# Kernel tuning notes

Hardware: AMD Instinct MI355X
Metric: run time of the kernel (lower is better)

## Reference

```python
import jax, jax.numpy as jnp
import numpy as np

NPOINT = 1024
RADIUS = 0.2
NSAMPLE = 32


def furthest_point_sampling(xyz, npoint):
    # xyz: (B, N, 3) -> (B, npoint) int32 indices
    B, N, _ = xyz.shape

    def step(carry, _):
        dist, far = carry
        centroid = jnp.take_along_axis(xyz, far[:, None, None], axis=1)  # (B,1,3)
        d = jnp.sum((xyz - centroid) ** 2, axis=-1)                       # (B,N)
        dist = jnp.minimum(dist, d)
        new_far = jnp.argmax(dist, axis=-1).astype(jnp.int32)
        return (dist, new_far), far

    init = (jnp.full((B, N), 1e10, xyz.dtype), jnp.zeros((B,), jnp.int32))
    _, idx = jax.lax.scan(step, init, None, length=npoint)
    return idx.T  # (B, npoint)


def ball_query(xyz, new_xyz, radius, nsample):
    # xyz: (B,N,3), new_xyz: (B,S,3) -> (B,S,nsample) int32 indices
    N = xyz.shape[1]
    d2 = jnp.sum((new_xyz[:, :, None, :] - xyz[:, None, :, :]) ** 2, axis=-1)  # (B,S,N)
    # pick first `nsample` indices within radius (CUDA ball_query semantics)
    key = jnp.where(d2 < radius * radius, jnp.arange(N, dtype=jnp.int32)[None, None, :], N)
    idx = jnp.sort(key, axis=-1)[..., :nsample]          # (B,S,nsample)
    first = idx[..., :1]
    idx = jnp.where(idx == N, first, idx)                # pad with first valid
    return jnp.clip(idx, 0, N - 1).astype(jnp.int32)     # guard empty balls


def sa_forward(xyz, features, W1, s1, b1, W2, s2, b2, W3, s3, b3):
    B, N, _ = xyz.shape
    center_idx = furthest_point_sampling(xyz, NPOINT)                     # (B,S)
    new_xyz = jnp.take_along_axis(xyz, center_idx[..., None], axis=1)     # (B,S,3)

    idx = ball_query(xyz, new_xyz, RADIUS, NSAMPLE)                       # (B,S,K)
    # group xyz (relative coords) and features
    g_xyz = jnp.take_along_axis(xyz[:, None], idx[..., None], axis=2)     # (B,S,K,3)
    g_xyz = g_xyz - new_xyz[:, :, None, :]
    feats_n = jnp.swapaxes(features, 1, 2)                                # (B,N,C)
    g_feat = jnp.take_along_axis(feats_n[:, None], idx[..., None], axis=2)  # (B,S,K,C)
    g = jnp.concatenate([g_xyz, g_feat], axis=-1)                         # (B,S,K,3+C)
    x = jnp.transpose(g, (0, 3, 1, 2))                                    # (B,3+C,S,K)

    # 1x1 conv MLP with (folded) BN affine + ReLU
    for W, s, b in ((W1, s1, b1), (W2, s2, b2), (W3, s3, b3)):
        x = jax.nn.relu(jnp.einsum('oi,bisk->bosk', W, x)
                        * s[None, :, None, None] + b[None, :, None, None])
    new_features = jnp.max(x, axis=-1)                                    # (B,Cout,S)
    return new_xyz, new_features


def setup_inputs() -> dict:
    key = jax.random.key(0)
    ks = jax.random.split(key, 11)
    B, N, C = 4, 16384, 64
    return {
        'xyz': jax.random.uniform(ks[0], (B, N, 3), jnp.float32),
        'features': jax.random.normal(ks[1], (B, C, N), jnp.float32),
        'W1': jax.random.normal(ks[2], (64, C + 3), jnp.float32) * 0.1,
        's1': jax.random.uniform(ks[3], (64,), jnp.float32),
        'b1': jax.random.normal(ks[4], (64,), jnp.float32) * 0.1,
        'W2': jax.random.normal(ks[5], (64, 64), jnp.float32) * 0.1,
        's2': jax.random.uniform(ks[6], (64,), jnp.float32),
        'b2': jax.random.normal(ks[7], (64,), jnp.float32) * 0.1,
        'W3': jax.random.normal(ks[8], (128, 64), jnp.float32) * 0.1,
        's3': jax.random.uniform(ks[9], (128,), jnp.float32),
        'b3': jax.random.normal(ks[10], (128,), jnp.float32) * 0.1,
    }


def reference(xyz, features, W1, s1, b1, W2, s2, b2, W3, s3, b3):
    return sa_forward(xyz, features, W1, s1, b1, W2, s2, b2, W3, s3, b3)
```

## Files before the change

### kernel.cpp

```cpp
#include <hip/hip_runtime.h>
#include <cstdint>
#include <cstddef>

#define BATCH   4
#define NPTS    16384
#define NPOINT  1024
#define NSAMPLE 32
#define CIN     67
#define R2f     0.04f

#define FPS_T   512
#define FPS_P   32

#define RPT32(M) M(0)M(1)M(2)M(3)M(4)M(5)M(6)M(7)M(8)M(9)M(10)M(11)M(12)M(13)M(14)M(15) \
                 M(16)M(17)M(18)M(19)M(20)M(21)M(22)M(23)M(24)M(25)M(26)M(27)M(28)M(29)M(30)M(31)

template <int CTRL, int RMASK>
__device__ __forceinline__ void amax_dpp(float& v, int& i) {
  int nv = __builtin_amdgcn_update_dpp(__float_as_int(v), __float_as_int(v),
                                       CTRL, RMASK, 0xf, false);
  int ni = __builtin_amdgcn_update_dpp(i, i, CTRL, RMASK, 0xf, false);
  float fv = __int_as_float(nv);
  bool tk = (fv > v) || (fv == v && ni < i);
  v = tk ? fv : v;
  i = tk ? ni : i;
}

__global__ void __attribute__((amdgpu_flat_work_group_size(FPS_T, FPS_T),
                               amdgpu_waves_per_eu(2, 2)))
fps_kernel(const float* __restrict__ xyz, float* __restrict__ out_newxyz)
{
  const int b = blockIdx.x;
  const float* base = xyz + (size_t)b * NPTS * 3;
  const int t = threadIdx.x;
  const int lane = t & 63, w = t >> 6;

#define DECLV(i) float px##i, py##i, pz##i, dd##i;
  RPT32(DECLV)
#undef DECLV
#define LOADV(i) { const float* p = base + (size_t)(((i) << 9) + t) * 3; \
                   px##i = p[0]; py##i = p[1]; pz##i = p[2]; dd##i = 1e10f; }
  RPT32(LOADV)
#undef LOADV

  __shared__ float s_wv[2][8];
  __shared__ int   s_wi[2][8];

  float cx = base[0], cy = base[1], cz = base[2];

  for (int it = 0; it < NPOINT; ++it) {
    if (t == 0) {
      int o = (b * NPOINT + it) * 3;
      out_newxyz[o + 0] = cx;
      out_newxyz[o + 1] = cy;
      out_newxyz[o + 2] = cz;
    }
    float bv = -1.0f; int bl = 0;
#define STEPV(i) { \
    float dx = __fsub_rn(px##i, cx); \
    float dy = __fsub_rn(py##i, cy); \
    float dz = __fsub_rn(pz##i, cz); \
    float d2 = __fadd_rn(__fadd_rn(__fmul_rn(dx, dx), __fmul_rn(dy, dy)), \
                         __fmul_rn(dz, dz)); \
    float nd = fminf(dd##i, d2); dd##i = nd; \
    bool tk = nd > bv;   \
    bv = tk ? nd : bv; \
    bl = tk ? (i) : bl; }
    RPT32(STEPV)
#undef STEPV
    int bi = (bl << 9) + t;

    amax_dpp<0x121, 0xf>(bv, bi);
    amax_dpp<0x122, 0xf>(bv, bi);
    amax_dpp<0x124, 0xf>(bv, bi);
    amax_dpp<0x128, 0xf>(bv, bi);
    amax_dpp<0x142, 0xa>(bv, bi);
    amax_dpp<0x143, 0xc>(bv, bi);

    const int par = it & 1;
    if (lane == 63) { s_wv[par][w] = bv; s_wi[par][w] = bi; }
    __syncthreads();

    float gv = s_wv[par][lane & 7];
    int   gi = s_wi[par][lane & 7];
    amax_dpp<0x121, 0xf>(gv, gi);
    amax_dpp<0x122, 0xf>(gv, gi);
    amax_dpp<0x124, 0xf>(gv, gi);

    int far = __builtin_amdgcn_readfirstlane(gi);
    cx = base[far * 3 + 0];
    cy = base[far * 3 + 1];
    cz = base[far * 3 + 2];
  }
}

__global__ __launch_bounds__(256) void transpose_kernel(
    const float* __restrict__ f, float* __restrict__ ft)
{
  __shared__ float tile[64][65];
  int b  = blockIdx.x >> 8;
  int n0 = (blockIdx.x & 255) << 6;
  for (int v = threadIdx.x; v < 64 * 64; v += 256) {
    int c = v >> 6, j = v & 63;
    tile[c][j] = f[((size_t)(b * 64 + c)) * NPTS + n0 + j];
  }
  __syncthreads();
  for (int v = threadIdx.x; v < 64 * 64; v += 256) {
    int j = v >> 6, c = v & 63;
    ft[((size_t)(b * NPTS + n0 + j)) * 64 + c] = tile[c][j];
  }
}

__global__ __launch_bounds__(1024) void mlp_kernel(
    const float* __restrict__ xyz,
    const float* __restrict__ feats,
    const float* __restrict__ featsT,
    const float* __restrict__ nx,
    const float* __restrict__ W1, const float* __restrict__ s1, const float* __restrict__ b1,
    const float* __restrict__ W2, const float* __restrict__ s2, const float* __restrict__ b2,
    const float* __restrict__ W3, const float* __restrict__ s3, const float* __restrict__ b3,
    float* __restrict__ outF)
{
  __shared__ float W1t[CIN * 64];
  __shared__ float W2t[64 * 64];
  __shared__ float sb[512];
  __shared__ float xs[CIN * 34];
  __shared__ float h1[64 * 34];
  __shared__ float h2[64 * 34];
  __shared__ int   hm[128];
  __shared__ int   lid8[8][NSAMPLE];

  const int tid = threadIdx.x;
  const int lane = tid & 63, w = tid >> 6;

  for (int v = tid; v < CIN * 64; v += 1024) {
    int o = v / CIN, i = v - o * CIN;
    W1t[i * 64 + o] = W1[v];
  }
  for (int v = tid; v < 64 * 64; v += 1024) {
    int o = v >> 6, i = v & 63;
    W2t[i * 64 + o] = W2[v];
  }
  if (tid < 64)       sb[tid]       = s1[tid];
  else if (tid < 128) sb[tid]       = b1[tid - 64];
  else if (tid < 192) sb[tid]       = s2[tid - 128];
  else if (tid < 256) sb[tid]       = b2[tid - 192];
  else if (tid < 384) sb[tid]       = s3[tid - 256];
  else if (tid < 512) sb[tid]       = b3[tid - 384];

  if (w < 8) {
    int g = (blockIdx.x << 3) + w;
    int b = g >> 10;
    const float* base = xyz + (size_t)b * NPTS * 3;
    float cx = nx[g * 3 + 0], cy = nx[g * 3 + 1], cz = nx[g * 3 + 2];
    int cnt = 0, fidx = -1;
    for (int c0 = 0; c0 < NPTS && cnt < NSAMPLE; c0 += 64) {
      int i = c0 + lane;
      float dx = __fsub_rn(base[i * 3 + 0], cx);
      float dy = __fsub_rn(base[i * 3 + 1], cy);
      float dz = __fsub_rn(base[i * 3 + 2], cz);
      float d2 = __fadd_rn(__fadd_rn(__fmul_rn(dx, dx), __fmul_rn(dy, dy)),
                           __fmul_rn(dz, dz));
      bool pred = d2 < R2f;
      unsigned long long mk = __ballot(pred);
      if (pred) {
        int rank = cnt + __popcll(mk & ((1ull << lane) - 1ull));
        if (rank < NSAMPLE) lid8[w][rank] = i;
        if (rank == 0) fidx = i;
      }
      cnt += __popcll(mk);
    }
#pragma unroll
    for (int off = 32; off >= 1; off >>= 1) {
      int o = __shfl_xor(fidx, off);
      fidx = o > fidx ? o : fidx;
    }
    if (lane >= cnt && lane < NSAMPLE) lid8[w][lane] = fidx;
  }
  __syncthreads();

  for (int ci = 0; ci < 8; ++ci) {
    int g = (blockIdx.x << 3) + ci;
    int b = g >> 10, m = g & 1023;

    {
      int k = tid >> 5, c0 = tid & 31;
      int id = lid8[ci][k];
      for (int c = c0; c < CIN; c += 32) {
        float val;
        if (c < 3)
          val = __fsub_rn(xyz[((size_t)b * NPTS + id) * 3 + c], nx[g * 3 + c]);
        else if (featsT)
          val = featsT[((size_t)b * NPTS + id) * 64 + (c - 3)];
        else
          val = feats[((size_t)(b * 64 + (c - 3))) * NPTS + id];
        xs[c * 34 + k] = val;
      }
      if (tid < 128) hm[tid] = 0;
    }
    __syncthreads();

    {
      int oc = tid & 63, k0 = (tid >> 6) << 1;
      float a0 = 0.f, a1 = 0.f;
#pragma unroll 4
      for (int i = 0; i < CIN; ++i) {
        float ww = W1t[i * 64 + oc];
        a0 = fmaf(ww, xs[i * 34 + k0], a0);
        a1 = fmaf(ww, xs[i * 34 + k0 + 1], a1);
      }
      float s = sb[oc], bb = sb[64 + oc];
      h1[oc * 34 + k0]     = fmaxf(fmaf(a0, s, bb), 0.f);
      h1[oc * 34 + k0 + 1] = fmaxf(fmaf(a1, s, bb), 0.f);
    }
    __syncthreads();

    {
      int oc = tid & 63, k0 = (tid >> 6) << 1;
      float a0 = 0.f, a1 = 0.f;
#pragma unroll 4
      for (int i = 0; i < 64; ++i) {
        float ww = W2t[i * 64 + oc];
        a0 = fmaf(ww, h1[i * 34 + k0], a0);
        a1 = fmaf(ww, h1[i * 34 + k0 + 1], a1);
      }
      float s = sb[128 + oc], bb = sb[192 + oc];
      h2[oc * 34 + k0]     = fmaxf(fmaf(a0, s, bb), 0.f);
      h2[oc * 34 + k0 + 1] = fmaxf(fmaf(a1, s, bb), 0.f);
    }
    __syncthreads();

    {
      int oc = tid & 127, k0 = (tid >> 7) << 2;
      const float4* W3v = reinterpret_cast<const float4*>(W3);
      float a0 = 0.f, a1 = 0.f, a2 = 0.f, a3 = 0.f;
#pragma unroll 4
      for (int i4 = 0; i4 < 16; ++i4) {
        float4 wv = W3v[oc * 16 + i4];
        const float* hr = &h2[(i4 * 4) * 34 + k0];
        a0 = fmaf(wv.x, hr[0], a0); a1 = fmaf(wv.x, hr[1], a1);
        a2 = fmaf(wv.x, hr[2], a2); a3 = fmaf(wv.x, hr[3], a3);
        hr += 34;
        a0 = fmaf(wv.y, hr[0], a0); a1 = fmaf(wv.y, hr[1], a1);
        a2 = fmaf(wv.y, hr[2], a2); a3 = fmaf(wv.y, hr[3], a3);
        hr += 34;
        a0 = fmaf(wv.z, hr[0], a0); a1 = fmaf(wv.z, hr[1], a1);
        a2 = fmaf(wv.z, hr[2], a2); a3 = fmaf(wv.z, hr[3], a3);
        hr += 34;
        a0 = fmaf(wv.w, hr[0], a0); a1 = fmaf(wv.w, hr[1], a1);
        a2 = fmaf(wv.w, hr[2], a2); a3 = fmaf(wv.w, hr[3], a3);
      }
      float s = sb[256 + oc], bb = sb[384 + oc];
      float v0 = fmaxf(fmaf(a0, s, bb), 0.f);
      float v1 = fmaxf(fmaf(a1, s, bb), 0.f);
      float v2 = fmaxf(fmaf(a2, s, bb), 0.f);
      float v3 = fmaxf(fmaf(a3, s, bb), 0.f);
      float mv = fmaxf(fmaxf(v0, v1), fmaxf(v2, v3));
      atomicMax(&hm[oc], __float_as_int(mv));
    }
    __syncthreads();

    if (tid < 128)
      outF[(((size_t)b * 128 + tid) << 10) + m] = __int_as_float(hm[tid]);
    __syncthreads();
  }
}

extern "C" void kernel_launch(void* const* d_in, const int* in_sizes, int n_in,
                              void* d_out, int out_size, void* d_ws, size_t ws_size,
                              hipStream_t stream)
{
  if (n_in < 11) return;
  const float* xyz   = (const float*)d_in[0];
  const float* feats = (const float*)d_in[1];
  const float* W1 = (const float*)d_in[2];
  const float* s1 = (const float*)d_in[3];
  const float* b1 = (const float*)d_in[4];
  const float* W2 = (const float*)d_in[5];
  const float* s2 = (const float*)d_in[6];
  const float* b2 = (const float*)d_in[7];
  const float* W3 = (const float*)d_in[8];
  const float* s3 = (const float*)d_in[9];
  const float* b3 = (const float*)d_in[10];
  float* out = (float*)d_out;

  float* featsT = nullptr;
  size_t needT = (size_t)BATCH * NPTS * 64 * sizeof(float);
  if (ws_size >= needT) featsT = (float*)d_ws;

  fps_kernel<<<BATCH, FPS_T, 0, stream>>>(xyz, out);
  if (featsT) transpose_kernel<<<BATCH * 256, 256, 0, stream>>>(feats, featsT);
  mlp_kernel<<<512, 1024, 0, stream>>>(xyz, feats, featsT, out,
                                       W1, s1, b1, W2, s2, b2, W3, s3, b3,
                                       out + BATCH * NPOINT * 3);
}
```

Baseline: 2.267 ms.

## Move FPS x/y coordinates to LDS and vectorize distance math with packed float2

The FPS kernel no longer keeps all 32 points' x/y/z/dist in registers. It stores x and y in padded shared memory and keeps z and the running distance as float2 register pairs, computing distances with packed 2-wide vector ops. This is meant to cut VGPR pressure (waves_per_eu pinning is dropped) and use packed FP32 instructions to halve the arithmetic instruction count. In exchange it adds LDS reads every iteration and changes the per-thread argmax into a pairwise compare that must keep tie-breaking consistent.

```diff
diff --git a/kernel.cpp b/kernel.cpp
--- a/kernel.cpp
+++ b/kernel.cpp
@@ -1,6 +1,8 @@
 #include <hip/hip_runtime.h>
 #include <cstdint>
 #include <cstddef>
+
+#pragma clang fp contract(off)
 
 #define BATCH   4
 #define NPTS    16384
@@ -10,10 +12,11 @@
 #define R2f     0.04f
 
 #define FPS_T   512
-#define FPS_P   32
-
-#define RPT32(M) M(0)M(1)M(2)M(3)M(4)M(5)M(6)M(7)M(8)M(9)M(10)M(11)M(12)M(13)M(14)M(15) \
-                 M(16)M(17)M(18)M(19)M(20)M(21)M(22)M(23)M(24)M(25)M(26)M(27)M(28)M(29)M(30)M(31)
+#define FPS_PAD 34
+
+#define RPT16(M) M(0)M(1)M(2)M(3)M(4)M(5)M(6)M(7)M(8)M(9)M(10)M(11)M(12)M(13)M(14)M(15)
+
+typedef float v2f __attribute__((ext_vector_type(2)));
 
 template <int CTRL, int RMASK>
 __device__ __forceinline__ void amax_dpp(float& v, int& i) {
@@ -26,48 +29,71 @@
   i = tk ? ni : i;
 }
 
-__global__ void __attribute__((amdgpu_flat_work_group_size(FPS_T, FPS_T),
-                               amdgpu_waves_per_eu(2, 2)))
+__global__ void __launch_bounds__(FPS_T)
 fps_kernel(const float* __restrict__ xyz, float* __restrict__ out_newxyz)
 {
+  __shared__ float px[FPS_T * FPS_PAD];
+  __shared__ float py[FPS_T * FPS_PAD];
+  __shared__ float s_wv[2][8];
+  __shared__ int   s_wi[2][8];
+
   const int b = blockIdx.x;
   const float* base = xyz + (size_t)b * NPTS * 3;
   const int t = threadIdx.x;
   const int lane = t & 63, w = t >> 6;
-
-#define DECLV(i) float px##i, py##i, pz##i, dd##i;
-  RPT32(DECLV)
-#undef DECLV
-#define LOADV(i) { const float* p = base + (size_t)(((i) << 9) + t) * 3; \
-                   px##i = p[0]; py##i = p[1]; pz##i = p[2]; dd##i = 1e10f; }
-  RPT32(LOADV)
-#undef LOADV
-
-  __shared__ float s_wv[2][8];
-  __shared__ int   s_wi[2][8];
+  const int t34 = t * FPS_PAD;
+
+#define INITP(j) v2f pz##j, dd##j; { \
+    const float* p0 = base + (size_t)(((2*(j)) << 9) + t) * 3; \
+    const float* p1 = base + (size_t)(((2*(j)+1) << 9) + t) * 3; \
+    px[t34 + 2*(j)]     = p0[0];  px[t34 + 2*(j) + 1] = p1[0]; \
+    py[t34 + 2*(j)]     = p0[1];  py[t34 + 2*(j) + 1] = p1[1]; \
+    pz##j.x = p0[2];  pz##j.y = p1[2]; \
+    dd##j.x = 1e10f;  dd##j.y = 1e10f; }
+  RPT16(INITP)
+#undef INITP
 
   float cx = base[0], cy = base[1], cz = base[2];
 
   for (int it = 0; it < NPOINT; ++it) {
+#define PINJ(j) asm volatile("" : "+v"(pz##j), "+v"(dd##j));
+    RPT16(PINJ)
+#undef PINJ
+
     if (t == 0) {
       int o = (b * NPOINT + it) * 3;
       out_newxyz[o + 0] = cx;
       out_newxyz[o + 1] = cy;
       out_newxyz[o + 2] = cz;
     }
+
+    v2f cx2, cy2, cz2;
+    cx2.x = cx; cx2.y = cx;
+    cy2.x = cy; cy2.y = cy;
+    cz2.x = cz; cz2.y = cz;
+
     float bv = -1.0f; int bl = 0;
-#define STEPV(i) { \
-    float dx = __fsub_rn(px##i, cx); \
-    float dy = __fsub_rn(py##i, cy); \
-    float dz = __fsub_rn(pz##i, cz); \
-    float d2 = __fadd_rn(__fadd_rn(__fmul_rn(dx, dx), __fmul_rn(dy, dy)), \
-                         __fmul_rn(dz, dz)); \
-    float nd = fminf(dd##i, d2); dd##i = nd; \
-    bool tk = nd > bv;   \
-    bv = tk ? nd : bv; \
-    bl = tk ? (i) : bl; }
-    RPT32(STEPV)
-#undef STEPV
+#define STEP2(j) { \
+    v2f xx = *reinterpret_cast<const v2f*>(&px[t34 + 2*(j)]); \
+    v2f yy = *reinterpret_cast<const v2f*>(&py[t34 + 2*(j)]); \
+    v2f dx = xx - cx2; \
+    v2f dy = yy - cy2; \
+    v2f dz = pz##j - cz2; \
+    v2f sx = dx * dx; \
+    v2f sy = dy * dy; \
+    v2f sz = dz * dz; \
+    v2f d2 = (sx + sy) + sz; \
+    v2f nd; \
+    nd.x = fminf(dd##j.x, d2.x); \
+    nd.y = fminf(dd##j.y, d2.y); \
+    dd##j = nd; \
+    float m = fmaxf(nd.x, nd.y); \
+    int kw = (nd.x >= nd.y) ? (2*(j)) : (2*(j)+1);   \
+    bool tk = m > bv;                                \
+    bv = tk ? m : bv; \
+    bl = tk ? kw : bl; }
+    RPT16(STEP2)
+#undef STEP2
     int bi = (bl << 9) + t;
 
     amax_dpp<0x121, 0xf>(bv, bi);
```

Result: no change. 2.283 ms (+0.7%).
